# Optimization experiments

Measured on AMD Instinct MI355X. Metric: run time of the kernel, lower is better.

## Reference

```python
import jax, jax.numpy as jnp
import numpy as np
from jax import lax

B, N, C = 8, 16384, 128
HEADS, FF, KS = 8, 3.0, 5
HD = C // HEADS

def setup_inputs() -> dict:
    key = jax.random.key(0)
    ks = jax.random.split(key, 10)
    r = lambda k, s, sc=0.02: jax.random.normal(k, s, dtype=jnp.float32) * sc
    return {
        "x": jax.random.normal(ks[0], (B, N, C), dtype=jnp.float32),
        "Wq": r(ks[1], (C, C)),
        "Wkv": r(ks[2], (C, C)),
        "Wproj": r(ks[3], (C, C)),
        "bproj": jnp.zeros((C,), jnp.float32),
        "w_g": jax.random.normal(ks[4], (C, 1), dtype=jnp.float32),
        "scale": r(ks[5], (1, 1, C), 0.1),
        "pos_enc": r(ks[6], (1, N, C), 0.02),
        "dwc_w": r(ks[7], (HD, 1, KS, KS), 0.1),
        "dwc_b": jnp.zeros((HD,), jnp.float32),
        "H": 128,
        "W": 128,
    }

def _l2(a, axis):
    return jnp.sqrt(jnp.sum(a * a, axis=axis, keepdims=True))

def reference(x, Wq, Wkv, Wproj, bproj, w_g, scale, pos_enc, dwc_w, dwc_b, H, W):
    b, n_tok, c = x.shape
    scale_factor = HD ** (-0.5)
    q = x @ Wq.T                      # (B,N,C)
    k = x @ Wkv.T + pos_enc           # (B,N,C)  sr_ratio=1 path
    s = jax.nn.softplus(scale)
    q = (jax.nn.relu(q) + 1e-6) / s
    k = (jax.nn.relu(k) + 1e-6) / s
    qn, kn = _l2(q, -1), _l2(k, -1)
    q = q ** FF
    k = k ** FF
    q = q / _l2(q, -1) * qn
    k = k / _l2(k, -1) * kn
    A = (q @ w_g) * scale_factor      # (B,N,1)
    A = A / jnp.maximum(_l2(A, 1), 1e-12)  # F.normalize over dim=1
    G = jnp.sum(A * q, axis=1)        # (B,C)
    xg = G[:, None, :] * k            # (B,N,C)
    qh = q.reshape(b, n_tok, HEADS, HD).transpose(0, 2, 1, 3)  # (B,h,N,d)
    kh = k.reshape(b, n_tok, HEADS, HD).transpose(0, 2, 1, 3)
    z = 1.0 / (jnp.einsum('bhnd,bhd->bhn', qh, kh.mean(axis=2)) + 1e-6)
    xh = xg.reshape(b, n_tok, HEADS, HD).transpose(0, 2, 1, 3) * z[..., None]
    xo = xh.transpose(0, 2, 1, 3).reshape(b, n_tok, c)
    # faithful second transpose+reshape (memory reinterpretation in the source)
    xo = xo.transpose(0, 2, 1).reshape(b, n_tok, c)
    kimg = kh.reshape(b * HEADS, H, W, HD).transpose(0, 3, 1, 2)  # (B*h,d,H,W)
    pad = KS // 2
    conv = lax.conv_general_dilated(kimg, dwc_w, (1, 1), [(pad, pad), (pad, pad)],
                                    dimension_numbers=('NCHW', 'OIHW', 'NCHW'),
                                    feature_group_count=HD)
    conv = conv + dwc_b[None, :, None, None]
    xo = xo + conv.reshape(b, c, n_tok).transpose(0, 2, 1)
    return xo @ Wproj.T + bproj
```

## Files before the change

kernel.cpp:

```cpp
#include <hip/hip_runtime.h>
#include <hip/hip_bf16.h>

#define BB 8
#define NN 16384
#define CC 128

typedef __attribute__((ext_vector_type(8))) short bf16x8;
typedef __attribute__((ext_vector_type(4))) short short4v;
typedef __attribute__((ext_vector_type(4))) float f32x4;

__device__ __forceinline__ unsigned short f2bf(float f) {
    union { float f; unsigned u; } v; v.f = f;
    unsigned r = v.u + 0x7fffu + ((v.u >> 16) & 1u);
    return (unsigned short)(r >> 16);
}
__device__ __forceinline__ float bf2f(unsigned short h) {
    union { unsigned u; float f; } v; v.u = ((unsigned)h) << 16;
    return v.f;
}
__device__ __forceinline__ void split_trunc(float f, short& hi, short& lo) {
    union { float f; unsigned u; } v; v.f = f;
    const unsigned short hu = (unsigned short)(v.u >> 16);
    union { unsigned u; float f; } hf; hf.u = ((unsigned)hu) << 16;
    union { float f; unsigned u; } r; r.f = f - hf.f;
    hi = (short)hu;
    lo = (short)(r.u >> 16);
}

__global__ __launch_bounds__(256) void wprep_kernel(
    const float* __restrict__ Wq, const float* __restrict__ Wkv,
    const float* __restrict__ Wp, const float* __restrict__ scale,
    unsigned short* __restrict__ whi, unsigned short* __restrict__ wlo,
    float* __restrict__ sps)
{
    const int bid = blockIdx.x;
    if (bid == 48) {
        if (threadIdx.x < 128)
            sps[threadIdx.x] = 1.f / log1pf(expf(scale[threadIdx.x]));
        return;
    }
    const int mat = bid >> 4;
    const float* src = (mat == 0) ? Wq : ((mat == 1) ? Wkv : Wp);
    const int off = (bid & 15) * 1024 + threadIdx.x * 4;
    const float4 v = *(const float4*)(src + off);
    float f[4] = {v.x, v.y, v.z, v.w};
    short4v hv, lv;
#pragma unroll
    for (int j = 0; j < 4; ++j) {
        short h, lo2;
        split_trunc(f[j], h, lo2);
        hv[j] = h; lv[j] = lo2;
    }
    *(short4v*)(whi + mat * 16384 + off) = hv;
    *(short4v*)(wlo + mat * 16384 + off) = lv;
}

__global__ __launch_bounds__(256, 2) void qproj_kernel(
    const float* __restrict__ x, const unsigned short* __restrict__ whi,
    const unsigned short* __restrict__ wlo, const float* __restrict__ w_g,
    const float* __restrict__ sps,
    unsigned short* __restrict__ qout, float* __restrict__ partial1)
{
    __shared__ __align__(16) char wsm[65536];
    __shared__ float wpart[4][132];
    __shared__ float apl[128];

    const int tid  = threadIdx.x;
    const int w    = tid >> 6;
    const int l    = tid & 63;
    const int blk  = blockIdx.x;
    const int tok0 = blk * 128;

    bf16x8 xh[2][4], xl[2][4];
#pragma unroll
    for (int n = 0; n < 2; ++n) {
        const int r = w * 32 + n * 16 + (l & 15);
        const float* rowp = x + (tok0 + r) * 128 + (l >> 4) * 8;
#pragma unroll
        for (int kt = 0; kt < 4; ++kt) {
            const f32x4 a = *(const f32x4*)(rowp + kt * 32);
            const f32x4 b = *(const f32x4*)(rowp + kt * 32 + 4);
            const float f[8] = {a[0], a[1], a[2], a[3], b[0], b[1], b[2], b[3]};
            bf16x8 hv, lv;
#pragma unroll
            for (int j = 0; j < 8; ++j) {
                short h, lo2;
                split_trunc(f[j], h, lo2);
                hv[j] = h; lv[j] = lo2;
            }
            xh[n][kt] = hv; xl[n][kt] = lv;
        }
    }

#pragma unroll
    for (int it = 0; it < 16; ++it) {
        const int flat = it * 256 + tid;
        const int arr  = flat >> 11;
        const int c    = (flat >> 4) & 127;
        const int g    = flat & 15;
        const unsigned short* src = (arr ? wlo : whi) + c * 128 + g * 8;
        const int dst = arr * 32768 + c * 256 + ((g * 16) ^ ((c & 7) << 4));
        *(bf16x8*)(wsm + dst) = *(const bf16x8*)src;
    }
    __syncthreads();

    const int crow = (l >> 4) * 4;
    f32x4 acc[8][2];
#pragma unroll
    for (int m = 0; m < 8; ++m)
#pragma unroll
        for (int n = 0; n < 2; ++n) acc[m][n] = (f32x4)0.f;

#pragma unroll
    for (int m = 0; m < 8; ++m) {
        const int c = m * 16 + (l & 15);
        const int sw = (c & 7) << 4;
        bf16x8 ah[4], al[4];
#pragma unroll
        for (int kt = 0; kt < 4; ++kt) {
            const int fo = c * 256 + ((kt * 64 + (l >> 4) * 16) ^ sw);
            ah[kt] = *(const bf16x8*)(wsm + fo);
            al[kt] = *(const bf16x8*)(wsm + 32768 + fo);
        }
#pragma unroll
        for (int n = 0; n < 2; ++n)
#pragma unroll
            for (int kt = 0; kt < 4; ++kt) {
                acc[m][n] = __builtin_amdgcn_mfma_f32_16x16x32_bf16(ah[kt], xh[n][kt], acc[m][n], 0, 0, 0);
                acc[m][n] = __builtin_amdgcn_mfma_f32_16x16x32_bf16(ah[kt], xl[n][kt], acc[m][n], 0, 0, 0);
                acc[m][n] = __builtin_amdgcn_mfma_f32_16x16x32_bf16(al[kt], xh[n][kt], acc[m][n], 0, 0, 0);
            }
    }
    __syncthreads();

#pragma unroll
    for (int m = 0; m < 8; ++m) {
        const float4 is4 = *(const float4*)(sps + m * 16 + crow);
        const float is[4] = {is4.x, is4.y, is4.z, is4.w};
#pragma unroll
        for (int n = 0; n < 2; ++n)
#pragma unroll
            for (int j = 0; j < 4; ++j)
                acc[m][n][j] = (fmaxf(acc[m][n][j], 0.f) + 1e-6f) * is[j];
    }
    float fqn[2];
#pragma unroll
    for (int n = 0; n < 2; ++n) {
        float s2 = 0.f, s6 = 0.f;
#pragma unroll
        for (int m = 0; m < 8; ++m)
#pragma unroll
            for (int j = 0; j < 4; ++j) {
                const float v = acc[m][n][j], v2 = v * v;
                s2 += v2; s6 += v2 * v2 * v2;
            }
        s2 += __shfl_xor(s2, 16); s6 += __shfl_xor(s6, 16);
        s2 += __shfl_xor(s2, 32); s6 += __shfl_xor(s6, 32);
        fqn[n] = sqrtf(s2 / s6);
    }
#pragma unroll
    for (int m = 0; m < 8; ++m)
#pragma unroll
        for (int n = 0; n < 2; ++n)
#pragma unroll
            for (int j = 0; j < 4; ++j) {
                const float v = acc[m][n][j];
                acc[m][n][j] = v * v * v * fqn[n];
            }
    float d0 = 0.f, d1 = 0.f;
#pragma unroll
    for (int m = 0; m < 8; ++m) {
        const float4 wgv = *(const float4*)(w_g + m * 16 + crow);
#pragma unroll
        for (int j = 0; j < 4; ++j) {
            const float wg = (j == 0) ? wgv.x : (j == 1) ? wgv.y : (j == 2) ? wgv.z : wgv.w;
            d0 += acc[m][0][j] * wg;
            d1 += acc[m][1][j] * wg;
        }
    }
    d0 += __shfl_xor(d0, 16); d0 += __shfl_xor(d0, 32);
    d1 += __shfl_xor(d1, 16); d1 += __shfl_xor(d1, 32);
    const float ap0 = 0.25f * d0, ap1 = 0.25f * d1;

    float ssa = ap0 * ap0 + ap1 * ap1;
    ssa += __shfl_xor(ssa, 1); ssa += __shfl_xor(ssa, 2);
    ssa += __shfl_xor(ssa, 4); ssa += __shfl_xor(ssa, 8);
    if (l == 0) wpart[w][128] = ssa;
    if (l < 16) { apl[w * 32 + l] = ap0; apl[w * 32 + 16 + l] = ap1; }

    float g4[4] = {0.f, 0.f, 0.f, 0.f};
#pragma unroll
    for (int n = 0; n < 2; ++n) {
        const int t = l & 15;
        const int rb = w * 8192 + t * 512;
#pragma unroll
        for (int m = 0; m < 8; ++m) {
            const int ad = rb + (((m * 16 + crow) * 4) ^ ((t & 7) << 4));
            *(f32x4*)(wsm + ad) = acc[m][n];
        }
        asm volatile("s_waitcnt lgkmcnt(0)" ::: "memory");
#pragma unroll
        for (int j = 0; j < 8; ++j) {
            const int fid = j * 64 + l;
            const int row = fid >> 5;
            const int c4  = fid & 31;
            const int rb3 = w * 8192 + row * 512;
            const f32x4 v = *(f32x4*)(wsm + rb3 + ((c4 * 16) ^ ((row & 7) << 4)));
            const float apv = apl[w * 32 + n * 16 + row];
            short4v qv;
#pragma unroll
            for (int i = 0; i < 4; ++i) {
                g4[i] += apv * v[i];
                qv[i] = (short)f2bf(v[i]);
            }
            *(short4v*)(qout + (tok0 + w * 32 + n * 16 + row) * 128 + c4 * 4) = qv;
        }
    }
#pragma unroll
    for (int i = 0; i < 4; ++i) g4[i] += __shfl_xor(g4[i], 32);
    if (l < 32) {
#pragma unroll
        for (int i = 0; i < 4; ++i) wpart[w][(l & 31) * 4 + i] = g4[i];
    }
    __syncthreads();
    float* pblk = partial1 + blk * 132;
    if (tid < 128)
        pblk[tid] = wpart[0][tid] + wpart[1][tid] + wpart[2][tid] + wpart[3][tid];
    else if (tid == 128)
        pblk[128] = wpart[0][128] + wpart[1][128] + wpart[2][128] + wpart[3][128];
}

__global__ __launch_bounds__(256, 2) void kproj_kernel(
    const float* __restrict__ x, const unsigned short* __restrict__ whi,
    const unsigned short* __restrict__ wlo,
    const float* __restrict__ sps, const float* __restrict__ pos_enc,
    unsigned short* __restrict__ ktout, float* __restrict__ partial2)
{
    __shared__ __align__(16) char wsm[65536];
    __shared__ float wpart[4][128];

    const int tid  = threadIdx.x;
    const int w    = tid >> 6;
    const int l    = tid & 63;
    const int blk  = blockIdx.x;
    const int tok0 = blk * 128;
    const int tokb = (blk & 127) * 128;

    bf16x8 xh[2][4], xl[2][4];
#pragma unroll
    for (int n = 0; n < 2; ++n) {
        const int r = w * 32 + n * 16 + (l & 15);
        const float* rowp = x + (tok0 + r) * 128 + (l >> 4) * 8;
#pragma unroll
        for (int kt = 0; kt < 4; ++kt) {
            const f32x4 a = *(const f32x4*)(rowp + kt * 32);
            const f32x4 b = *(const f32x4*)(rowp + kt * 32 + 4);
            const float f[8] = {a[0], a[1], a[2], a[3], b[0], b[1], b[2], b[3]};
            bf16x8 hv, lv;
#pragma unroll
            for (int j = 0; j < 8; ++j) {
                short h, lo2;
                split_trunc(f[j], h, lo2);
                hv[j] = h; lv[j] = lo2;
            }
            xh[n][kt] = hv; xl[n][kt] = lv;
        }
    }

#pragma unroll
    for (int it = 0; it < 16; ++it) {
        const int flat = it * 256 + tid;
        const int arr  = flat >> 11;
        const int c    = (flat >> 4) & 127;
        const int g    = flat & 15;
        const unsigned short* src = (arr ? wlo : whi) + 16384 + c * 128 + g * 8;
        const int dst = arr * 32768 + c * 256 + ((g * 16) ^ ((c & 7) << 4));
        *(bf16x8*)(wsm + dst) = *(const bf16x8*)src;
    }
    __syncthreads();

    const int crow = (l >> 4) * 4;
    f32x4 acc[8][2];
#pragma unroll
    for (int m = 0; m < 8; ++m)
#pragma unroll
        for (int n = 0; n < 2; ++n) acc[m][n] = (f32x4)0.f;

#pragma unroll
    for (int m = 0; m < 8; ++m) {
        const int c = m * 16 + (l & 15);
        const int sw = (c & 7) << 4;
        bf16x8 ah[4], al[4];
#pragma unroll
        for (int kt = 0; kt < 4; ++kt) {
            const int fo = c * 256 + ((kt * 64 + (l >> 4) * 16) ^ sw);
            ah[kt] = *(const bf16x8*)(wsm + fo);
            al[kt] = *(const bf16x8*)(wsm + 32768 + fo);
        }
#pragma unroll
        for (int n = 0; n < 2; ++n)
#pragma unroll
            for (int kt = 0; kt < 4; ++kt) {
                acc[m][n] = __builtin_amdgcn_mfma_f32_16x16x32_bf16(ah[kt], xh[n][kt], acc[m][n], 0, 0, 0);
                acc[m][n] = __builtin_amdgcn_mfma_f32_16x16x32_bf16(ah[kt], xl[n][kt], acc[m][n], 0, 0, 0);
                acc[m][n] = __builtin_amdgcn_mfma_f32_16x16x32_bf16(al[kt], xh[n][kt], acc[m][n], 0, 0, 0);
            }
    }
    __syncthreads();

#pragma unroll
    for (int m = 0; m < 8; ++m) {
        const float4 is4 = *(const float4*)(sps + m * 16 + crow);
        const float is[4] = {is4.x, is4.y, is4.z, is4.w};
#pragma unroll
        for (int n = 0; n < 2; ++n) {
            const int t = tokb + w * 32 + n * 16 + (l & 15);
            const float4 p = *(const float4*)(pos_enc + t * 128 + m * 16 + crow);
            const float pe[4] = {p.x, p.y, p.z, p.w};
#pragma unroll
            for (int j = 0; j < 4; ++j)
                acc[m][n][j] = (fmaxf(acc[m][n][j] + pe[j], 0.f) + 1e-6f) * is[j];
        }
    }
    float fkn[2];
#pragma unroll
    for (int n = 0; n < 2; ++n) {
        float s2 = 0.f, s6 = 0.f;
#pragma unroll
        for (int m = 0; m < 8; ++m)
#pragma unroll
            for (int j = 0; j < 4; ++j) {
                const float v = acc[m][n][j], v2 = v * v;
                s2 += v2; s6 += v2 * v2 * v2;
            }
        s2 += __shfl_xor(s2, 16); s6 += __shfl_xor(s6, 16);
        s2 += __shfl_xor(s2, 32); s6 += __shfl_xor(s6, 32);
        fkn[n] = sqrtf(s2 / s6);
    }
#pragma unroll
    for (int m = 0; m < 8; ++m)
#pragma unroll
        for (int n = 0; n < 2; ++n)
#pragma unroll
            for (int j = 0; j < 4; ++j) {
                const float v = acc[m][n][j];
                acc[m][n][j] = v * v * v * fkn[n];
            }
#pragma unroll
    for (int m = 0; m < 8; ++m)
#pragma unroll
        for (int j = 0; j < 4; ++j) {
            float s = acc[m][0][j] + acc[m][1][j];
            s += __shfl_xor(s, 1); s += __shfl_xor(s, 2);
            s += __shfl_xor(s, 4); s += __shfl_xor(s, 8);
            if ((l & 15) == 0) wpart[w][m * 16 + crow + j] = s;
        }

#pragma unroll
    for (int m = 0; m < 8; ++m)
#pragma unroll
        for (int n = 0; n < 2; ++n)
#pragma unroll
            for (int j = 0; j < 4; ++j) {
                const int ch = m * 16 + crow + j;
                const int tl = w * 32 + n * 16 + (l & 15);
                *(unsigned short*)(wsm + ch * 264 + tl * 2) = f2bf(acc[m][n][j]);
            }
    __syncthreads();
    {
        const int bb = blk >> 7;
        unsigned* ktp = (unsigned*)ktout;
#pragma unroll
        for (int it = 0; it < 32; ++it) {
            const int idx = it * 256 + tid;
            const int row = idx >> 6;
            const int col = idx & 63;
            const unsigned v = *(unsigned*)(wsm + row * 264 + col * 4);
            ktp[(size_t)(bb * 128 + row) * 8192 + (blk & 127) * 64 + col] = v;
        }
    }
    __syncthreads();
    if (tid < 128)
        partial2[blk * 128 + tid] = wpart[0][tid] + wpart[1][tid] +
                                    wpart[2][tid] + wpart[3][tid];
}

__global__ __launch_bounds__(256) void reduce_kernel(
    const float* __restrict__ partial1, const float* __restrict__ partial2,
    float* __restrict__ G, float* __restrict__ kbar)
{
    const int b = blockIdx.x;
    const int tid = threadIdx.x;
    __shared__ float tmp[4];

    float ssa = (tid < 128) ? partial1[(b * 128 + tid) * 132 + 128] : 0.f;
#pragma unroll
    for (int o = 32; o >= 1; o >>= 1) ssa += __shfl_xor(ssa, o);
    if ((tid & 63) == 0) tmp[tid >> 6] = ssa;
    __syncthreads();
    const float anorm = fmaxf(sqrtf(tmp[0] + tmp[1] + tmp[2] + tmp[3]), 1e-12f);
    const float inv_a = 1.f / anorm;

    if (tid < 128) {
        float g = 0.f;
        for (int t = 0; t < 128; ++t)
            g += partial1[(b * 128 + t) * 132 + tid];
        G[b * 128 + tid] = g * inv_a;
    } else {
        const int c2 = tid - 128;
        float s = 0.f;
        for (int t = 0; t < 128; ++t)
            s += partial2[(b * 128 + t) * 128 + c2];
        kbar[b * 128 + c2] = s * (1.f / 16384.f);
    }
}

__global__ __launch_bounds__(256) void z_kernel(
    const unsigned short* __restrict__ q, const float* __restrict__ kbar,
    float* __restrict__ z)
{
    const int bid = blockIdx.x;
    const int b   = bid >> 8;
    const int tg  = bid & 255;
    const int tid = threadIdx.x;
    const int t   = tid >> 2;
    const int qt  = tid & 3;
    const int tok = tg * 64 + t;

    const unsigned short* qp = q + ((size_t)b * NN + tok) * 128 + qt * 32;
    const float* kb = kbar + b * 128 + qt * 32;

    float dot0 = 0.f, dot1 = 0.f;
#pragma unroll
    for (int c = 0; c < 4; ++c) {
        const short4v q4a = *(const short4v*)(qp + c * 8);
        const short4v q4b = *(const short4v*)(qp + c * 8 + 4);
        const float4 k4a = *(const float4*)(kb + c * 8);
        const float4 k4b = *(const float4*)(kb + c * 8 + 4);
        float d = bf2f((unsigned short)q4a[0]) * k4a.x + bf2f((unsigned short)q4a[1]) * k4a.y +
                  bf2f((unsigned short)q4a[2]) * k4a.z + bf2f((unsigned short)q4a[3]) * k4a.w +
                  bf2f((unsigned short)q4b[0]) * k4b.x + bf2f((unsigned short)q4b[1]) * k4b.y +
                  bf2f((unsigned short)q4b[2]) * k4b.z + bf2f((unsigned short)q4b[3]) * k4b.w;
        if (c < 2) dot0 += d; else dot1 += d;
    }
    z[((size_t)b * 8 + qt * 2) * NN + tok]     = 1.f / (dot0 + 1e-6f);
    z[((size_t)b * 8 + qt * 2 + 1) * NN + tok] = 1.f / (dot1 + 1e-6f);
}

__global__ __launch_bounds__(256, 2) void scp_kernel(
    float* __restrict__ out, const unsigned short* __restrict__ kt,
    const float* __restrict__ z, const float* __restrict__ G,
    const unsigned short* __restrict__ whi, const unsigned short* __restrict__ wlo,
    const float* __restrict__ bp, const float* __restrict__ dwc_w,
    const float* __restrict__ dwc_b)
{
    __shared__ __align__(16) char smem[32768];
    __shared__ float wct[25][16];
    __shared__ float bi[16];
    __shared__ float Gs;

    const int tid  = threadIdx.x;
    const int bid0 = blockIdx.x;
    const int bid  = (bid0 & 7) * 128 + (bid0 >> 3);
    const int cc   = bid & 127;
    const int b    = bid >> 7;
    const int n0   = bid * 128;

    for (int i = tid; i < 400; i += 256)
        wct[i >> 4][i & 15] = dwc_w[(i & 15) * 25 + (i >> 4)];
    if (tid < 16) bi[tid] = dwc_b[tid];
    if (tid == 0) Gs = G[b * 128 + cc];
    __syncthreads();

    const int ch4 = tid >> 3;
    const int xg  = tid & 7;

    float acc[4][16];
#pragma unroll
    for (int c = 0; c < 4; ++c)
#pragma unroll
        for (int i = 0; i < 16; ++i) acc[c][i] = 0.f;

#pragma unroll
    for (int dy = 0; dy < 5; ++dy) {
        const int yy = cc + dy - 2;
        if (yy < 0 || yy > 127) continue;
#pragma unroll
        for (int c = 0; c < 4; ++c) {
            const int ch = ch4 * 4 + c;
            const unsigned short* rowp = kt + ((size_t)b * 128 + ch) * NN
                                            + yy * 128 + xg * 16 - 8;
            float wf[32];
#pragma unroll
            for (int q4 = 0; q4 < 4; ++q4) {
                const bf16x8 v = *(const bf16x8*)(rowp + q4 * 8);
#pragma unroll
                for (int e = 0; e < 8; ++e)
                    wf[q4 * 8 + e] = bf2f((unsigned short)v[e]);
            }
            if (xg == 0) {
#pragma unroll
                for (int e = 0; e < 8; ++e) wf[e] = 0.f;
            }
            if (xg == 7) {
#pragma unroll
                for (int e = 24; e < 32; ++e) wf[e] = 0.f;
            }
            const int d = ch & 15;
#pragma unroll
            for (int dx = 0; dx < 5; ++dx) {
                const float wv = wct[dy * 5 + dx][d];
#pragma unroll
                for (int i = 0; i < 16; ++i)
                    acc[c][i] += wv * wf[i + dx + 6];
            }
        }
    }

    const float Gcc = Gs;
    const unsigned short* kub = kt + ((size_t)b * 128 + cc) * NN;
    const float* zr = z + ((size_t)b * 8 + (cc >> 4)) * NN;
    const int dbase = (ch4 & 3) * 4;
    const float4 b4 = *(const float4*)(&bi[dbase]);
    const float bv[4] = {b4.x, b4.y, b4.z, b4.w};
#pragma unroll
    for (int i = 0; i < 16; ++i) {
        const int r = xg * 16 + i;
        const int toks = r * 128 + ch4 * 4;
        const short4v ku4 = *(const short4v*)(kub + toks);
        const float4 z4 = *(const float4*)(zr + toks);
        const float zz[4] = {z4.x, z4.y, z4.z, z4.w};
        short4v hv;
#pragma unroll
        for (int c = 0; c < 4; ++c) {
            const float f = Gcc * bf2f((unsigned short)ku4[c]) * zz[c] + acc[c][i] + bv[c];
            hv[c] = (short)f2bf(f);
        }
        const int ad = r * 256 + (((ch4 >> 1) * 16) ^ ((r & 7) << 4)) + (ch4 & 1) * 8;
        *(short4v*)(smem + ad) = hv;
    }
    __syncthreads();

    const int w  = tid >> 6;
    const int ll = tid & 63;
    bf16x8 xh[2][4];
    {
        const int lg16 = (ll >> 4) * 16;
#pragma unroll
        for (int n = 0; n < 2; ++n) {
            const int r = w * 32 + n * 16 + (ll & 15);
            const int rb = r * 256;
            const int sw = (r & 7) << 4;
#pragma unroll
            for (int kt2 = 0; kt2 < 4; ++kt2)
                xh[n][kt2] = *(bf16x8*)(smem + rb + ((kt2 * 64 + lg16) ^ sw));
        }
    }
    const int crow = (ll >> 4) * 4;
    f32x4 pacc[8][2];
#pragma unroll
    for (int m = 0; m < 8; ++m)
#pragma unroll
        for (int n = 0; n < 2; ++n) pacc[m][n] = (f32x4)0.f;

#pragma unroll
    for (int m = 0; m < 8; ++m) {
        const int c = m * 16 + (ll & 15);
        bf16x8 ah[4], al[4];
#pragma unroll
        for (int kt2 = 0; kt2 < 4; ++kt2) {
            const int off = 32768 + c * 128 + kt2 * 32 + (ll >> 4) * 8;
            ah[kt2] = *(const bf16x8*)(whi + off);
            al[kt2] = *(const bf16x8*)(wlo + off);
        }
#pragma unroll
        for (int n = 0; n < 2; ++n)
#pragma unroll
            for (int kt2 = 0; kt2 < 4; ++kt2) {
                pacc[m][n] = __builtin_amdgcn_mfma_f32_16x16x32_bf16(ah[kt2], xh[n][kt2], pacc[m][n], 0, 0, 0);
                pacc[m][n] = __builtin_amdgcn_mfma_f32_16x16x32_bf16(al[kt2], xh[n][kt2], pacc[m][n], 0, 0, 0);
            }
    }

#pragma unroll
    for (int m = 0; m < 8; ++m) {
        const float4 bq = *(const float4*)(bp + m * 16 + crow);
        const float bb[4] = {bq.x, bq.y, bq.z, bq.w};
#pragma unroll
        for (int n = 0; n < 2; ++n)
#pragma unroll
            for (int j = 0; j < 4; ++j) pacc[m][n][j] += bb[j];
    }
    __syncthreads();
#pragma unroll
    for (int n = 0; n < 2; ++n) {
        const int t = ll & 15;
        const int rb = w * 8192 + t * 512;
#pragma unroll
        for (int m = 0; m < 8; ++m) {
            const int ad = rb + (((m * 16 + crow) * 4) ^ ((t & 7) << 4));
            *(f32x4*)(smem + ad) = pacc[m][n];
        }
        asm volatile("s_waitcnt lgkmcnt(0)" ::: "memory");
#pragma unroll
        for (int j = 0; j < 8; ++j) {
            const int fid = j * 64 + ll;
            const int row = fid >> 5;
            const int c4  = fid & 31;
            const int rb3 = w * 8192 + row * 512;
            const f32x4 v = *(f32x4*)(smem + rb3 + ((c4 * 16) ^ ((row & 7) << 4)));
            *(f32x4*)(out + (n0 + w * 32 + n * 16 + row) * 128 + c4 * 4) = v;
        }
    }
}

extern "C" void kernel_launch(void* const* d_in, const int* in_sizes, int n_in,
                              void* d_out, int out_size, void* d_ws, size_t ws_size,
                              hipStream_t stream)
{
    const float* x       = (const float*)d_in[0];
    const float* Wq      = (const float*)d_in[1];
    const float* Wkv     = (const float*)d_in[2];
    const float* Wproj   = (const float*)d_in[3];
    const float* bproj   = (const float*)d_in[4];
    const float* w_g     = (const float*)d_in[5];
    const float* scale   = (const float*)d_in[6];
    const float* pos_enc = (const float*)d_in[7];
    const float* dwc_w   = (const float*)d_in[8];
    const float* dwc_b   = (const float*)d_in[9];
    float* out = (float*)d_out;

    char* ws = (char*)d_ws;
    unsigned short* qbuf = (unsigned short*)(ws);
    unsigned short* ktbuf= (unsigned short*)(ws + 33554432);
    float* partial1 = (float*)(ws + 67108864);
    float* partial2 = (float*)(ws + 67649536);
    float* G        = (float*)(ws + 68173824);
    float* kbar     = (float*)(ws + 68177920);
    unsigned short* whi = (unsigned short*)(ws + 68182016);
    unsigned short* wlo = (unsigned short*)(ws + 68280320);
    float* sps      = (float*)(ws + 68378624);
    float* zbuf     = (float*)(ws + 68379136);

    wprep_kernel<<<dim3(49), dim3(256), 0, stream>>>(
        Wq, Wkv, Wproj, scale, whi, wlo, sps);
    qproj_kernel<<<dim3(1024), dim3(256), 0, stream>>>(
        x, whi, wlo, w_g, sps, qbuf, partial1);
    kproj_kernel<<<dim3(1024), dim3(256), 0, stream>>>(
        x, whi, wlo, sps, pos_enc, ktbuf, partial2);
    reduce_kernel<<<dim3(8), dim3(256), 0, stream>>>(
        partial1, partial2, G, kbar);
    z_kernel<<<dim3(2048), dim3(256), 0, stream>>>(qbuf, kbar, zbuf);
    scp_kernel<<<dim3(1024), dim3(256), 0, stream>>>(
        out, ktbuf, zbuf, G, whi, wlo, bproj, dwc_w, dwc_b);
}
```

Measured before the change: 169.4 us.

## Split scp_kernel tiles in half and raise occupancy to three blocks per CU

The final conv+projection kernel now handles 64 tokens per block instead of 128, doubling the grid to 2048 blocks and halving per-thread accumulators, conv window loads and MFMA accumulators. Launch bounds rise to 3 blocks per CU, and the LDS swizzle is adjusted for the new row mapping. The aim is more parallelism and better latency hiding from lower register pressure. In exchange, more halo rows are reloaded across blocks and per-block setup (weight tables, whi/wlo loads) is amortised over less work.

```diff
diff --git a/kernel.cpp b/kernel.cpp
--- a/kernel.cpp
+++ b/kernel.cpp
@@ -447,7 +447,7 @@
     z[((size_t)b * 8 + qt * 2 + 1) * NN + tok] = 1.f / (dot1 + 1e-6f);
 }
 
-__global__ __launch_bounds__(256, 2) void scp_kernel(
+__global__ __launch_bounds__(256, 3) void scp_kernel(
     float* __restrict__ out, const unsigned short* __restrict__ kt,
     const float* __restrict__ z, const float* __restrict__ G,
     const unsigned short* __restrict__ whi, const unsigned short* __restrict__ wlo,
@@ -461,10 +461,11 @@
 
     const int tid  = threadIdx.x;
     const int bid0 = blockIdx.x;
-    const int bid  = (bid0 & 7) * 128 + (bid0 >> 3);
-    const int cc   = bid & 127;
-    const int b    = bid >> 7;
-    const int n0   = bid * 128;
+    const int bid  = (bid0 & 7) * 256 + (bid0 >> 3);
+    const int b    = bid >> 8;
+    const int cc   = (bid & 255) >> 1;
+    const int half = bid & 1;
+    const int n0   = b * NN + cc * 128 + half * 64;
 
     for (int i = tid; i < 400; i += 256)
         wct[i >> 4][i & 15] = dwc_w[(i & 15) * 25 + (i >> 4)];
@@ -474,12 +475,13 @@
 
     const int ch4 = tid >> 3;
     const int xg  = tid & 7;
-
-    float acc[4][16];
+    const int x0  = half * 64 + xg * 8;
+
+    float acc[4][8];
 #pragma unroll
     for (int c = 0; c < 4; ++c)
 #pragma unroll
-        for (int i = 0; i < 16; ++i) acc[c][i] = 0.f;
+        for (int i = 0; i < 8; ++i) acc[c][i] = 0.f;
 
 #pragma unroll
     for (int dy = 0; dy < 5; ++dy) {
@@ -489,29 +491,29 @@
         for (int c = 0; c < 4; ++c) {
             const int ch = ch4 * 4 + c;
             const unsigned short* rowp = kt + ((size_t)b * 128 + ch) * NN
-                                            + yy * 128 + xg * 16 - 8;
-            float wf[32];
-#pragma unroll
-            for (int q4 = 0; q4 < 4; ++q4) {
+                                            + yy * 128 + x0 - 8;
+            float wf[24];
+#pragma unroll
+            for (int q4 = 0; q4 < 3; ++q4) {
                 const bf16x8 v = *(const bf16x8*)(rowp + q4 * 8);
 #pragma unroll
                 for (int e = 0; e < 8; ++e)
                     wf[q4 * 8 + e] = bf2f((unsigned short)v[e]);
             }
-            if (xg == 0) {
+            if (x0 == 0) {
 #pragma unroll
                 for (int e = 0; e < 8; ++e) wf[e] = 0.f;
             }
-            if (xg == 7) {
-#pragma unroll
-                for (int e = 24; e < 32; ++e) wf[e] = 0.f;
+            if (x0 == 120) {
+#pragma unroll
+                for (int e = 16; e < 24; ++e) wf[e] = 0.f;
             }
             const int d = ch & 15;
 #pragma unroll
             for (int dx = 0; dx < 5; ++dx) {
                 const float wv = wct[dy * 5 + dx][d];
 #pragma unroll
-                for (int i = 0; i < 16; ++i)
+                for (int i = 0; i < 8; ++i)
                     acc[c][i] += wv * wf[i + dx + 6];
             }
         }
@@ -524,9 +526,9 @@
     const float4 b4 = *(const float4*)(&bi[dbase]);
     const float bv[4] = {b4.x, b4.y, b4.z, b4.w};
 #pragma unroll
-    for (int i = 0; i < 16; ++i) {
-        const int r = xg * 16 + i;
-        const int toks = r * 128 + ch4 * 4;
+    for (int i = 0; i < 8; ++i) {
+        const int rl = xg * 8 + i;
+        const int toks = (x0 + i) * 128 + ch4 * 4;
         const short4v ku4 = *(const short4v*)(kub + toks);
         const float4 z4 = *(const float4*)(zr + toks);
         const float zz[4] = {z4.x, z4.y, z4.z, z4.w};
@@ -536,32 +538,27 @@
             const float f = Gcc * bf2f((unsigned short)ku4[c]) * zz[c] + acc[c][i] + bv[c];
             hv[c] = (short)f2bf(f);
         }
-        const int ad = r * 256 + (((ch4 >> 1) * 16) ^ ((r & 7) << 4)) + (ch4 & 1) * 8;
+        const int swz = (((rl & 7) ^ ((rl >> 3) & 7)) << 4);
+        const int ad = rl * 256 + (((ch4 >> 1) * 16) ^ swz) + (ch4 & 1) * 8;
         *(short4v*)(smem + ad) = hv;
     }
     __syncthreads();
 
     const int w  = tid >> 6;
     const int ll = tid & 63;
-    bf16x8 xh[2][4];
+    bf16x8 xh[4];
     {
         const int lg16 = (ll >> 4) * 16;
-#pragma unroll
-        for (int n = 0; n < 2; ++n) {
-            const int r = w * 32 + n * 16 + (ll & 15);
-            const int rb = r * 256;
-            const int sw = (r & 7) << 4;
-#pragma unroll
-            for (int kt2 = 0; kt2 < 4; ++kt2)
-                xh[n][kt2] = *(bf16x8*)(smem + rb + ((kt2 * 64 + lg16) ^ sw));
-        }
+        const int r = w * 16 + (ll & 15);
+        const int swz = (((r & 7) ^ ((r >> 3) & 7)) << 4);
+#pragma unroll
+        for (int kt2 = 0; kt2 < 4; ++kt2)
+            xh[kt2] = *(bf16x8*)(smem + r * 256 + ((kt2 * 64 + lg16) ^ swz));
     }
     const int crow = (ll >> 4) * 4;
-    f32x4 pacc[8][2];
-#pragma unroll
-    for (int m = 0; m < 8; ++m)
-#pragma unroll
-        for (int n = 0; n < 2; ++n) pacc[m][n] = (f32x4)0.f;
+    f32x4 pacc[8];
+#pragma unroll
+    for (int m = 0; m < 8; ++m) pacc[m] = (f32x4)0.f;
 
 #pragma unroll
     for (int m = 0; m < 8; ++m) {
@@ -574,32 +571,29 @@
             al[kt2] = *(const bf16x8*)(wlo + off);
         }
 #pragma unroll
-        for (int n = 0; n < 2; ++n)
-#pragma unroll
-            for (int kt2 = 0; kt2 < 4; ++kt2) {
-                pacc[m][n] = __builtin_amdgcn_mfma_f32_16x16x32_bf16(ah[kt2], xh[n][kt2], pacc[m][n], 0, 0, 0);
-                pacc[m][n] = __builtin_amdgcn_mfma_f32_16x16x32_bf16(al[kt2], xh[n][kt2], pacc[m][n], 0, 0, 0);
-            }
+        for (int kt2 = 0; kt2 < 4; ++kt2) {
+            pacc[m] = __builtin_amdgcn_mfma_f32_16x16x32_bf16(ah[kt2], xh[kt2], pacc[m], 0, 0, 0);
+            pacc[m] = __builtin_amdgcn_mfma_f32_16x16x32_bf16(al[kt2], xh[kt2], pacc[m], 0, 0, 0);
+        }
     }
 
 #pragma unroll
     for (int m = 0; m < 8; ++m) {
         const float4 bq = *(const float4*)(bp + m * 16 + crow);
-        const float bb[4] = {bq.x, bq.y, bq.z, bq.w};
-#pragma unroll
-        for (int n = 0; n < 2; ++n)
-#pragma unroll
-            for (int j = 0; j < 4; ++j) pacc[m][n][j] += bb[j];
-    }
-    __syncthreads();
-#pragma unroll
-    for (int n = 0; n < 2; ++n) {
+#pragma unroll
+        for (int j = 0; j < 4; ++j) {
+            const float bb = (j == 0) ? bq.x : (j == 1) ? bq.y : (j == 2) ? bq.z : bq.w;
+            pacc[m][j] += bb;
+        }
+    }
+    __syncthreads();
+    {
         const int t = ll & 15;
         const int rb = w * 8192 + t * 512;
 #pragma unroll
         for (int m = 0; m < 8; ++m) {
             const int ad = rb + (((m * 16 + crow) * 4) ^ ((t & 7) << 4));
-            *(f32x4*)(smem + ad) = pacc[m][n];
+            *(f32x4*)(smem + ad) = pacc[m];
         }
         asm volatile("s_waitcnt lgkmcnt(0)" ::: "memory");
 #pragma unroll
@@ -609,7 +603,7 @@
             const int c4  = fid & 31;
             const int rb3 = w * 8192 + row * 512;
             const f32x4 v = *(f32x4*)(smem + rb3 + ((c4 * 16) ^ ((row & 7) << 4)));
-            *(f32x4*)(out + (n0 + w * 32 + n * 16 + row) * 128 + c4 * 4) = v;
+            *(f32x4*)(out + (size_t)(n0 + w * 16 + row) * 128 + c4 * 4) = v;
         }
     }
 }
@@ -651,6 +645,6 @@
     reduce_kernel<<<dim3(8), dim3(256), 0, stream>>>(
         partial1, partial2, G, kbar);
     z_kernel<<<dim3(2048), dim3(256), 0, stream>>>(qbuf, kbar, zbuf);
-    scp_kernel<<<dim3(1024), dim3(256), 0, stream>>>(
+    scp_kernel<<<dim3(2048), dim3(256), 0, stream>>>(
         out, ktbuf, zbuf, G, whi, wlo, bproj, dwc_w, dwc_b);
 }
```

New measurement: 204.8 us. 1.21x slower.
